# Kernel tuning notes

Hardware: AMD Instinct MI355X
Metric: run time of the kernel (lower is better)

## Reference

```python
import jax, jax.numpy as jnp
import numpy as np

H, W = 512, 512          # image_shape
FH, FW = 64, 64          # filter_size
NUM_PARTS = 256
N = 8192                 # number of placed parts


def setup_inputs() -> dict:
    key = jax.random.key(0)
    k1, k2, k3, k4 = jax.random.split(key, 4)
    filters = jax.random.normal(k1, (NUM_PARTS, FH, FW), dtype=jnp.float32)
    part = jax.random.randint(k2, (N,), 0, NUM_PARTS)
    row = jax.random.randint(k3, (N,), 0, H)
    col = jax.random.randint(k4, (N,), 0, W)
    phw_list = jnp.stack([part, row, col], axis=1).astype(jnp.int32)  # [N,3]
    return {"phw_list": phw_list, "filters": filters}


def reference(phw_list, filters):
    # Original: for each part i, slice filters[part_idx] to the in-bounds window
    # and += into canvas[from_r:to_r, from_c:to_c].
    # Equivalent vectorized form: scatter-add FULL filters onto a padded canvas
    # (pad = full filter size on each side, so all writes are in-bounds), then
    # crop back to (H, W). Clipping via crop == the original's slice clipping.
    fo_h, fo_w = FH // 2, FW // 2  # filter center offsets
    part = phw_list[:, 0]
    row = phw_list[:, 1]
    col = phw_list[:, 2]

    filts = filters[part]                                  # (N, FH, FW) gather
    r0 = row - fo_h + FH                                   # top-left row in padded canvas
    c0 = col - fo_w + FW                                   # top-left col in padded canvas
    rr = r0[:, None, None] + jnp.arange(FH)[None, :, None]  # (N, FH, 1)
    cc = c0[:, None, None] + jnp.arange(FW)[None, None, :]  # (N, 1, FW)

    padded = jnp.zeros((H + 2 * FH, W + 2 * FW), dtype=filters.dtype)
    padded = padded.at[rr, cc].add(filts)                  # overlapping scatter-add
    return padded[FH:FH + H, FW:FW + W]                    # (H, W) canvas
```

## Files before the change

### kernel.cpp

```cpp
#include <hip/hip_runtime.h>


#define H_  512
#define W_  512
#define FH_ 64
#define FW_ 64
#define TILE_ 32
#define THREADS_ 256
#define SEG_LEN_ 1024
#define PLANE_   (H_ * W_)

__device__ __forceinline__ int clamp63(int v) {
    return min(max(v, 0), 63);
}

template<bool PLANES>
__global__ __launch_bounds__(THREADS_, 8)
void render_tile_kernel(const int* __restrict__ phw,
                        const float* __restrict__ filters,
                        float* __restrict__ dst,
                        int n) {
    __shared__ unsigned int s_list[SEG_LEN_];
    __shared__ int s_cnt;

    const int t   = threadIdx.x;
    const int tx0 = blockIdx.x * TILE_;
    const int ty0 = blockIdx.y * TILE_;
    const int k0  = blockIdx.z * SEG_LEN_;
    const int k1  = (k0 + SEG_LEN_ < n) ? (k0 + SEG_LEN_) : n;

    if (t == 0) s_cnt = 0;
    __syncthreads();

    for (int k = k0 + t; k < k1; k += THREADS_) {
        const int part = phw[k * 3 + 0];
        const int row  = phw[k * 3 + 1];
        const int col  = phw[k * 3 + 2];
        const bool hit =
            (row >= ty0 - (FH_ / 2 - 1)) && (row <= ty0 + TILE_ - 1 + FH_ / 2) &&
            (col >= tx0 - (FW_ / 2 - 1)) && (col <= tx0 + TILE_ - 1 + FW_ / 2);
        if (hit) {
            const int idx = atomicAdd(&s_cnt, 1);
            s_list[idx] = ((unsigned)part << 18) | ((unsigned)row << 9) | (unsigned)col;
        }
    }
    __syncthreads();
    const int cnt = s_cnt;

    const int xl    = t & 31;
    const int yb    = t >> 5;
    const int x     = tx0 + xl;
    const int ybase = ty0 + yb;

    float acc0 = 0.f, acc1 = 0.f, acc2 = 0.f, acc3 = 0.f;

    auto body = [&](unsigned v) {
        const int part = (int)__builtin_amdgcn_readfirstlane(v >> 18);
        const int row  = (int)__builtin_amdgcn_readfirstlane((v >> 9) & 511u);
        const int col  = (int)__builtin_amdgcn_readfirstlane(v & 511u);
        const float* __restrict__ f = filters + (part << 12);

        const int  j   = x - col + (FW_ / 2);
        const int  jc  = clamp63(j);
        const bool jok = (unsigned)j < (unsigned)FW_;
        const int  i0  = ybase - row + (FH_ / 2);

        const int ia = i0;      const int ib = i0 + 8;
        const int ic = i0 + 16; const int id = i0 + 24;
        const float va = f[clamp63(ia) * FW_ + jc];
        const float vb = f[clamp63(ib) * FW_ + jc];
        const float vc = f[clamp63(ic) * FW_ + jc];
        const float vd = f[clamp63(id) * FW_ + jc];
        acc0 += (jok && (unsigned)ia < (unsigned)FH_) ? va : 0.f;
        acc1 += (jok && (unsigned)ib < (unsigned)FH_) ? vb : 0.f;
        acc2 += (jok && (unsigned)ic < (unsigned)FH_) ? vc : 0.f;
        acc3 += (jok && (unsigned)id < (unsigned)FH_) ? vd : 0.f;
    };

    int k = 0;
    for (; k + 4 <= cnt; k += 4) {
        const uint4 vv = *(const uint4*)&s_list[k];
        body(vv.x); body(vv.y); body(vv.z); body(vv.w);
    }
    for (; k < cnt; ++k) body(s_list[k]);

    if constexpr (PLANES) {
        float* __restrict__ plane = dst + (size_t)blockIdx.z * PLANE_;
        plane[(ybase +  0) * W_ + x] = acc0;
        plane[(ybase +  8) * W_ + x] = acc1;
        plane[(ybase + 16) * W_ + x] = acc2;
        plane[(ybase + 24) * W_ + x] = acc3;
    } else {
        atomicAdd(&dst[(ybase +  0) * W_ + x], acc0);
        atomicAdd(&dst[(ybase +  8) * W_ + x], acc1);
        atomicAdd(&dst[(ybase + 16) * W_ + x], acc2);
        atomicAdd(&dst[(ybase + 24) * W_ + x], acc3);
    }
}

template<int SEGS>
__global__ __launch_bounds__(256)
void reduce_planes_fixed(const float* __restrict__ planes, float* __restrict__ out) {
    const int i = (blockIdx.x * 256 + threadIdx.x) * 4;
    float4 a = *(const float4*)&planes[i];
#pragma unroll
    for (int s = 1; s < SEGS; ++s) {
        const float4 b = *(const float4*)&planes[(size_t)s * PLANE_ + i];
        a.x += b.x; a.y += b.y; a.z += b.z; a.w += b.w;
    }
    *(float4*)&out[i] = a;
}

__global__ __launch_bounds__(256)
void reduce_planes_var(const float* __restrict__ planes, float* __restrict__ out,
                       int segs) {
    const int i = (blockIdx.x * 256 + threadIdx.x) * 4;
    float4 a = *(const float4*)&planes[i];
    for (int s = 1; s < segs; ++s) {
        const float4 b = *(const float4*)&planes[(size_t)s * PLANE_ + i];
        a.x += b.x; a.y += b.y; a.z += b.z; a.w += b.w;
    }
    *(float4*)&out[i] = a;
}

extern "C" void kernel_launch(void* const* d_in, const int* in_sizes, int n_in,
                              void* d_out, int out_size, void* d_ws, size_t ws_size,
                              hipStream_t stream) {
    const int*   phw     = (const int*)d_in[0];
    const float* filters = (const float*)d_in[1];
    float*       out     = (float*)d_out;
    const int n = in_sizes[0] / 3;

    if (n <= 0) {
        hipMemsetAsync(out, 0, (size_t)H_ * W_ * sizeof(float), stream);
        return;
    }

    const int segs = (n + SEG_LEN_ - 1) / SEG_LEN_;
    const size_t plane_bytes = (size_t)segs * PLANE_ * sizeof(float);
    dim3 grid(W_ / TILE_, H_ / TILE_, segs);

    if (d_ws != nullptr && ws_size >= plane_bytes) {
        float* planes = (float*)d_ws;
        render_tile_kernel<true><<<grid, dim3(THREADS_), 0, stream>>>(
            phw, filters, planes, n);
        const int rblocks = PLANE_ / 4 / 256;
        if (segs == 8) {
            reduce_planes_fixed<8><<<dim3(rblocks), dim3(256), 0, stream>>>(planes, out);
        } else {
            reduce_planes_var<<<dim3(rblocks), dim3(256), 0, stream>>>(planes, out, segs);
        }
    } else {
        hipMemsetAsync(out, 0, (size_t)H_ * W_ * sizeof(float), stream);
        render_tile_kernel<false><<<grid, dim3(THREADS_), 0, stream>>>(
            phw, filters, out, n);
    }
}
```

Baseline: 82.60 us.

## Fuse render and plane reduction via cooperative grid sync; skip dead filter rows per wave

Merges the render kernel and the plane reduction into one cooperative kernel. A grid-wide sync separates the two phases, so the second kernel launch and its gap disappear. It also adds wave-uniform range checks so each wave skips filter loads for accumulator rows that fall outside the placed filter. In exchange, all 2048 blocks must be co-resident, and a grid barrier plus threadfence are added. Occupancy is queried once and cached in a static variable.

```diff
diff --git a/kernel.cpp b/kernel.cpp
--- a/kernel.cpp
+++ b/kernel.cpp
@@ -1,4 +1,7 @@
 #include <hip/hip_runtime.h>
+#include <hip/hip_cooperative_groups.h>
+
+namespace cg = cooperative_groups;
 
 
 #define H_  512
@@ -8,28 +11,25 @@
 #define TILE_ 32
 #define THREADS_ 256
 #define SEG_LEN_ 1024
+#define SEGS_    8
 #define PLANE_   (H_ * W_)
 
 __device__ __forceinline__ int clamp63(int v) {
     return min(max(v, 0), 63);
 }
 
-template<bool PLANES>
-__global__ __launch_bounds__(THREADS_, 8)
-void render_tile_kernel(const int* __restrict__ phw,
-                        const float* __restrict__ filters,
-                        float* __restrict__ dst,
-                        int n) {
-    __shared__ unsigned int s_list[SEG_LEN_];
-    __shared__ int s_cnt;
-
+__device__ __forceinline__ void render_core(const int* __restrict__ phw,
+                                            const float* __restrict__ filters,
+                                            int n, unsigned* s_list, int* s_cnt,
+                                            float& acc0, float& acc1,
+                                            float& acc2, float& acc3) {
     const int t   = threadIdx.x;
     const int tx0 = blockIdx.x * TILE_;
     const int ty0 = blockIdx.y * TILE_;
     const int k0  = blockIdx.z * SEG_LEN_;
     const int k1  = (k0 + SEG_LEN_ < n) ? (k0 + SEG_LEN_) : n;
 
-    if (t == 0) s_cnt = 0;
+    if (t == 0) *s_cnt = 0;
     __syncthreads();
 
     for (int k = k0 + t; k < k1; k += THREADS_) {
@@ -40,19 +40,20 @@
             (row >= ty0 - (FH_ / 2 - 1)) && (row <= ty0 + TILE_ - 1 + FH_ / 2) &&
             (col >= tx0 - (FW_ / 2 - 1)) && (col <= tx0 + TILE_ - 1 + FW_ / 2);
         if (hit) {
-            const int idx = atomicAdd(&s_cnt, 1);
+            const int idx = atomicAdd(s_cnt, 1);
             s_list[idx] = ((unsigned)part << 18) | ((unsigned)row << 9) | (unsigned)col;
         }
     }
     __syncthreads();
-    const int cnt = s_cnt;
+    const int cnt = *s_cnt;
 
     const int xl    = t & 31;
     const int yb    = t >> 5;
     const int x     = tx0 + xl;
     const int ybase = ty0 + yb;
-
-    float acc0 = 0.f, acc1 = 0.f, acc2 = 0.f, acc3 = 0.f;
+    const int ybw   = (int)__builtin_amdgcn_readfirstlane(yb);
+
+    acc0 = 0.f; acc1 = 0.f; acc2 = 0.f; acc3 = 0.f;
 
     auto body = [&](unsigned v) {
         const int part = (int)__builtin_amdgcn_readfirstlane(v >> 18);
@@ -64,17 +65,27 @@
         const int  jc  = clamp63(j);
         const bool jok = (unsigned)j < (unsigned)FW_;
         const int  i0  = ybase - row + (FH_ / 2);
-
-        const int ia = i0;      const int ib = i0 + 8;
-        const int ic = i0 + 16; const int id = i0 + 24;
-        const float va = f[clamp63(ia) * FW_ + jc];
-        const float vb = f[clamp63(ib) * FW_ + jc];
-        const float vc = f[clamp63(ic) * FW_ + jc];
-        const float vd = f[clamp63(id) * FW_ + jc];
-        acc0 += (jok && (unsigned)ia < (unsigned)FH_) ? va : 0.f;
-        acc1 += (jok && (unsigned)ib < (unsigned)FH_) ? vb : 0.f;
-        acc2 += (jok && (unsigned)ic < (unsigned)FH_) ? vc : 0.f;
-        acc3 += (jok && (unsigned)id < (unsigned)FH_) ? vd : 0.f;
+        const int  A   = ty0 + ybw - row + (FH_ / 2);
+
+        if (A >=  -1 && A <= 63) {
+            const float va = f[clamp63(i0) * FW_ + jc];
+            acc0 += (jok && (unsigned)i0 < (unsigned)FH_) ? va : 0.f;
+        }
+        if (A >=  -9 && A <= 55) {
+            const int ib = i0 + 8;
+            const float vb = f[clamp63(ib) * FW_ + jc];
+            acc1 += (jok && (unsigned)ib < (unsigned)FH_) ? vb : 0.f;
+        }
+        if (A >= -17 && A <= 47) {
+            const int ic = i0 + 16;
+            const float vc = f[clamp63(ic) * FW_ + jc];
+            acc2 += (jok && (unsigned)ic < (unsigned)FH_) ? vc : 0.f;
+        }
+        if (A >= -25 && A <= 39) {
+            const int id = i0 + 24;
+            const float vd = f[clamp63(id) * FW_ + jc];
+            acc3 += (jok && (unsigned)id < (unsigned)FH_) ? vd : 0.f;
+        }
     };
 
     int k = 0;
@@ -83,32 +94,68 @@
         body(vv.x); body(vv.y); body(vv.z); body(vv.w);
     }
     for (; k < cnt; ++k) body(s_list[k]);
+}
+
+__global__ __launch_bounds__(THREADS_, 8)
+void render_coop(const int* __restrict__ phw, const float* __restrict__ filters,
+                 float* __restrict__ planes, float* __restrict__ out, int n) {
+    __shared__ unsigned s_list[SEG_LEN_];
+    __shared__ int s_cnt;
+
+    float a0, a1, a2, a3;
+    render_core(phw, filters, n, s_list, &s_cnt, a0, a1, a2, a3);
+
+    const int t     = threadIdx.x;
+    const int x     = blockIdx.x * TILE_ + (t & 31);
+    const int ybase = blockIdx.y * TILE_ + (t >> 5);
+    float* __restrict__ plane = planes + (size_t)blockIdx.z * PLANE_;
+    plane[(ybase +  0) * W_ + x] = a0;
+    plane[(ybase +  8) * W_ + x] = a1;
+    plane[(ybase + 16) * W_ + x] = a2;
+    plane[(ybase + 24) * W_ + x] = a3;
+
+    __threadfence();
+    cg::this_grid().sync();
+
+    if (blockIdx.z == 0) {
+        const int i = (((int)blockIdx.y * (int)gridDim.x + (int)blockIdx.x) * THREADS_ + t) * 4;
+        float4 a = *(const float4*)&planes[i];
+#pragma unroll
+        for (int s = 1; s < SEGS_; ++s) {
+            const float4 b = *(const float4*)&planes[(size_t)s * PLANE_ + i];
+            a.x += b.x; a.y += b.y; a.z += b.z; a.w += b.w;
+        }
+        *(float4*)&out[i] = a;
+    }
+}
+
+template<bool PLANES>
+__global__ __launch_bounds__(THREADS_, 8)
+void render_tile_kernel(const int* __restrict__ phw,
+                        const float* __restrict__ filters,
+                        float* __restrict__ dst, int n) {
+    __shared__ unsigned s_list[SEG_LEN_];
+    __shared__ int s_cnt;
+
+    float a0, a1, a2, a3;
+    render_core(phw, filters, n, s_list, &s_cnt, a0, a1, a2, a3);
+
+    const int t     = threadIdx.x;
+    const int x     = blockIdx.x * TILE_ + (t & 31);
+    const int ybase = blockIdx.y * TILE_ + (t >> 5);
 
     if constexpr (PLANES) {
         float* __restrict__ plane = dst + (size_t)blockIdx.z * PLANE_;
-        plane[(ybase +  0) * W_ + x] = acc0;
-        plane[(ybase +  8) * W_ + x] = acc1;
-        plane[(ybase + 16) * W_ + x] = acc2;
-        plane[(ybase + 24) * W_ + x] = acc3;
+        plane[(ybase +  0) * W_ + x] = a0;
+        plane[(ybase +  8) * W_ + x] = a1;
+        plane[(ybase + 16) * W_ + x] = a2;
+        plane[(ybase + 24) * W_ + x] = a3;
     } else {
-        atomicAdd(&dst[(ybase +  0) * W_ + x], acc0);
-        atomicAdd(&dst[(ybase +  8) * W_ + x], acc1);
-        atomicAdd(&dst[(ybase + 16) * W_ + x], acc2);
-        atomicAdd(&dst[(ybase + 24) * W_ + x], acc3);
-    }
-}
-
-template<int SEGS>
-__global__ __launch_bounds__(256)
-void reduce_planes_fixed(const float* __restrict__ planes, float* __restrict__ out) {
-    const int i = (blockIdx.x * 256 + threadIdx.x) * 4;
-    float4 a = *(const float4*)&planes[i];
-#pragma unroll
-    for (int s = 1; s < SEGS; ++s) {
-        const float4 b = *(const float4*)&planes[(size_t)s * PLANE_ + i];
-        a.x += b.x; a.y += b.y; a.z += b.z; a.w += b.w;
-    }
-    *(float4*)&out[i] = a;
+        atomicAdd(&dst[(ybase +  0) * W_ + x], a0);
+        atomicAdd(&dst[(ybase +  8) * W_ + x], a1);
+        atomicAdd(&dst[(ybase + 16) * W_ + x], a2);
+        atomicAdd(&dst[(ybase + 24) * W_ + x], a3);
+    }
 }
 
 __global__ __launch_bounds__(256)
@@ -140,16 +187,30 @@
     const size_t plane_bytes = (size_t)segs * PLANE_ * sizeof(float);
     dim3 grid(W_ / TILE_, H_ / TILE_, segs);
 
-    if (d_ws != nullptr && ws_size >= plane_bytes) {
+    static int coop_ok = -1;
+    if (coop_ok < 0) {
+        int blocksPerCU = 0, numCU = 0;
+        hipError_t e1 = hipOccupancyMaxActiveBlocksPerMultiprocessor(
+            &blocksPerCU, (const void*)render_coop, THREADS_, 0);
+        hipDeviceProp_t prop;
+        hipError_t e2 = hipGetDeviceProperties(&prop, 0);
+        numCU = prop.multiProcessorCount;
+        coop_ok = (e1 == hipSuccess && e2 == hipSuccess &&
+                   (long)blocksPerCU * numCU >= (long)grid.x * grid.y * SEGS_) ? 1 : 0;
+    }
+
+    if (d_ws != nullptr && ws_size >= plane_bytes && segs == SEGS_ && coop_ok == 1) {
+        float* planes = (float*)d_ws;
+        void* args[] = {(void*)&phw, (void*)&filters, (void*)&planes,
+                        (void*)&out, (void*)&n};
+        hipLaunchCooperativeKernel((const void*)render_coop, grid,
+                                   dim3(THREADS_), args, 0, stream);
+    } else if (d_ws != nullptr && ws_size >= plane_bytes) {
         float* planes = (float*)d_ws;
         render_tile_kernel<true><<<grid, dim3(THREADS_), 0, stream>>>(
             phw, filters, planes, n);
         const int rblocks = PLANE_ / 4 / 256;
-        if (segs == 8) {
-            reduce_planes_fixed<8><<<dim3(rblocks), dim3(256), 0, stream>>>(planes, out);
-        } else {
-            reduce_planes_var<<<dim3(rblocks), dim3(256), 0, stream>>>(planes, out, segs);
-        }
+        reduce_planes_var<<<dim3(rblocks), dim3(256), 0, stream>>>(planes, out, segs);
     } else {
         hipMemsetAsync(out, 0, (size_t)H_ * W_ * sizeof(float), stream);
         render_tile_kernel<false><<<grid, dim3(THREADS_), 0, stream>>>(
```

Result: slower. 105.4 us (+27.7%).
